# Kernel optimization log

Measured on AMD Instinct MI355X. Metric: run time of the kernel, lower is better.

## Reference

```python
import jax, jax.numpy as jnp
import numpy as np

N_NODES = 32
N_HEADS = 4
HEAD_DIM = 64
NEG_SLOPE = 0.2  # PyG GATConv default LeakyReLU slope


def setup_inputs() -> dict:
    key = jax.random.key(0)
    ks = jax.random.split(key, 8)
    roi_feats = jax.random.normal(ks[0], (N_NODES, 256, 96, 96), dtype=jnp.float32)
    edge_index = jax.random.randint(ks[1], (2, 512), 0, N_NODES, dtype=jnp.int32)
    W = jax.random.normal(ks[2], (256, N_HEADS * HEAD_DIM), dtype=jnp.float32) * 0.0625
    a_src = jax.random.normal(ks[3], (N_HEADS, HEAD_DIM), dtype=jnp.float32) * 0.125
    a_dst = jax.random.normal(ks[4], (N_HEADS, HEAD_DIM), dtype=jnp.float32) * 0.125
    gat_bias = jnp.zeros((N_HEADS * HEAD_DIM,), dtype=jnp.float32)
    cls_W = jax.random.normal(ks[5], (256, 32), dtype=jnp.float32) * 0.0625
    cls_b = jnp.zeros((32,), dtype=jnp.float32)
    return {"roi_feats": roi_feats, "edge_index": edge_index, "W": W,
            "a_src": a_src, "a_dst": a_dst, "gat_bias": gat_bias,
            "cls_W": cls_W, "cls_b": cls_b}


def _gat_conv(x, edge_index, W, a_src, a_dst, bias):
    # x: [N, C]; edge_index: [2, E] (src row 0, dst row 1)
    N = x.shape[0]
    # PyG GATConv adds self-loops by default
    loops = jnp.arange(N, dtype=edge_index.dtype)
    src = jnp.concatenate([edge_index[0], loops])
    dst = jnp.concatenate([edge_index[1], loops])
    h = (x @ W).reshape(N, N_HEADS, HEAD_DIM)          # [N, H, F]
    alpha_s = jnp.einsum('nhf,hf->nh', h, a_src)       # [N, H]
    alpha_d = jnp.einsum('nhf,hf->nh', h, a_dst)
    e = alpha_s[src] + alpha_d[dst]                    # [E', H]
    e = jnp.where(e >= 0, e, NEG_SLOPE * e)            # LeakyReLU
    # segment softmax over incoming edges of each dst node
    m = jax.ops.segment_max(e, dst, num_segments=N)    # [N, H]
    ex = jnp.exp(e - m[dst])
    denom = jax.ops.segment_sum(ex, dst, num_segments=N)
    alpha = ex / denom[dst]                            # [E', H]
    out = jax.ops.segment_sum(alpha[:, :, None] * h[src], dst, num_segments=N)
    return out.reshape(N, N_HEADS * HEAD_DIM) + bias


def reference(roi_feats, edge_index, W, a_src, a_dst, gat_bias, cls_W, cls_b):
    # [N, C, H, W] -> [N, C] spatial mean pool
    x = roi_feats.mean(axis=(2, 3))
    x = _gat_conv(x, edge_index, W, a_src, a_dst, gat_bias)
    logit = jax.nn.silu(x) @ cls_W + cls_b             # [N, num_au]
    return logit
```

## Files before the change

### kernel.cpp

```cpp
#include <hip/hip_runtime.h>
#include <math.h>

#define N_NODES  32
#define N_HEADS  4
#define HEAD_DIM 64
#define CDIM     256
#define HWPIX    9216
#define ROWF4    2304
#define E_BASE   512
#define E_TOT    544
#define NEG_SLOPE 0.2f
#define XS       257

__global__ __launch_bounds__(256, 4) void pool_kernel(const float* __restrict__ roi,
                                                      float* __restrict__ x) {
    const int wave = threadIdx.x >> 6, lane = threadIdx.x & 63;
    const int row = blockIdx.x * 4 + wave;
    const float4* p = reinterpret_cast<const float4*>(roi) + (size_t)row * ROWF4 + lane;

    float4 A[12], B[12];
    float s = 0.f;

#pragma unroll
    for (int j = 0; j < 12; ++j) A[j] = p[j * 64];
#pragma unroll
    for (int j = 0; j < 12; ++j) B[j] = p[(12 + j) * 64];
#pragma unroll
    for (int j = 0; j < 12; ++j) s += (A[j].x + A[j].y) + (A[j].z + A[j].w);
#pragma unroll
    for (int j = 0; j < 12; ++j) A[j] = p[(24 + j) * 64];
#pragma unroll
    for (int j = 0; j < 12; ++j) s += (B[j].x + B[j].y) + (B[j].z + B[j].w);
#pragma unroll
    for (int j = 0; j < 12; ++j) s += (A[j].x + A[j].y) + (A[j].z + A[j].w);

#pragma unroll
    for (int off = 32; off; off >>= 1) s += __shfl_down(s, off);
    if (lane == 0) x[row] = s * (1.0f / (float)HWPIX);
}

__global__ __launch_bounds__(256) void gat_kernel(const int* __restrict__ edge_index,
                                                  const float* __restrict__ x,
                                                  const float* __restrict__ W,
                                                  const float* __restrict__ a_src,
                                                  const float* __restrict__ a_dst,
                                                  const float* __restrict__ gat_bias,
                                                  const float* __restrict__ cls_W,
                                                  const float* __restrict__ cls_b,
                                                  float* __restrict__ out) {
    const int n = blockIdx.x;
    const int t = threadIdx.x;
    const int wavg = t >> 6, lane = t & 63;

    __shared__ float    xs[N_NODES * XS];
    __shared__ __align__(16) float asl[CDIM];
    __shared__ __align__(16) float adl[CDIM];
    __shared__ float    was[CDIM * N_HEADS];
    __shared__ float    wad[CDIM * N_HEADS];
    __shared__ float    als[N_NODES * N_HEADS];
    __shared__ float    adn[N_HEADS];
    __shared__ unsigned msegu[N_HEADS];
    __shared__ float    dseg[N_HEADS];
    __shared__ float    M[N_NODES * N_HEADS];
    __shared__ float    y[N_HEADS * CDIM];
    __shared__ float    sv[CDIM];
    __shared__ float4   red4[N_HEADS][64];
    __shared__ float    cred[8][32];

    float4 xv[8];
#pragma unroll
    for (int k = 0; k < 8; ++k) xv[k] = ((const float4*)x)[t + k * 256];
    const float asr = a_src[t], adr = a_dst[t];
    const int es0 = edge_index[t],       ed0 = edge_index[E_BASE + t];
    const int es1 = edge_index[256 + t], ed1 = edge_index[E_BASE + 256 + t];
    float4 bias4 = make_float4(0.f, 0.f, 0.f, 0.f);
    if (t < 64) bias4 = ((const float4*)gat_bias)[t];
    float cb = 0.f;
    if (t < 32) cb = cls_b[t];

#pragma unroll
    for (int k = 0; k < 8; ++k) {
        const int i = (t + k * 256) * 4, s = i >> 8, c = i & 255;
        xs[s * XS + c + 0] = xv[k].x;
        xs[s * XS + c + 1] = xv[k].y;
        xs[s * XS + c + 2] = xv[k].z;
        xs[s * XS + c + 3] = xv[k].w;
    }
    asl[t] = asr;
    adl[t] = adr;
    if (t < 128) M[t] = 0.f;
    if (t < 4) { msegu[t] = 0u; dseg[t] = 0.f; }
    __syncthreads();

    {
        float accs[4] = {0.f, 0.f, 0.f, 0.f};
        float accd[4] = {0.f, 0.f, 0.f, 0.f};
        const float4* wr  = (const float4*)(W + (size_t)t * CDIM);
        const float4* as4 = (const float4*)asl;
        const float4* ad4 = (const float4*)adl;
#pragma unroll 32
        for (int j = 0; j < 64; ++j) {
            const float4 w = wr[j], av = as4[j], dv = ad4[j];
            const int hd = j >> 4;
            accs[hd] += w.x * av.x + w.y * av.y + w.z * av.z + w.w * av.w;
            accd[hd] += w.x * dv.x + w.y * dv.y + w.z * dv.z + w.w * dv.w;
        }
#pragma unroll
        for (int hd = 0; hd < 4; ++hd) {
            was[t * 4 + hd] = accs[hd];
            wad[t * 4 + hd] = accd[hd];
        }
    }
    __syncthreads();

    if (t < 132) {
        if (t < 128) {
            const int s = t >> 2, hd = t & 3;
            const float* xrow = &xs[s * XS];
            float acc = 0.f;
#pragma unroll 8
            for (int c = 0; c < CDIM; ++c) acc += xrow[c] * was[c * 4 + hd];
            als[t] = acc;
        } else {
            const int hd = t - 128;
            const float* xrow = &xs[n * XS];
            float acc = 0.f;
#pragma unroll 8
            for (int c = 0; c < CDIM; ++c) acc += xrow[c] * wad[c * 4 + hd];
            adn[hd] = acc;
        }
    }
    __syncthreads();

    {
        const bool sl = (t < 32) && (t == n);
#pragma unroll
        for (int hd = 0; hd < 4; ++hd) {
            float best = -INFINITY;
            if (ed0 == n) {
                float v = als[es0 * 4 + hd] + adn[hd];
                best = fmaxf(best, (v >= 0.f) ? v : NEG_SLOPE * v);
            }
            if (ed1 == n) {
                float v = als[es1 * 4 + hd] + adn[hd];
                best = fmaxf(best, (v >= 0.f) ? v : NEG_SLOPE * v);
            }
            if (sl) {
                float v = als[n * 4 + hd] + adn[hd];
                best = fmaxf(best, (v >= 0.f) ? v : NEG_SLOPE * v);
            }
            if (best > -INFINITY) {
                const int iv = __float_as_int(best);
                const unsigned key = (iv < 0) ? ~(unsigned)iv
                                              : ((unsigned)iv | 0x80000000u);
                atomicMax(&msegu[hd], key);
            }
        }
    }
    __syncthreads();

    float mx[4];
#pragma unroll
    for (int hd = 0; hd < 4; ++hd) {
        const unsigned key = msegu[hd];
        const int im = (key & 0x80000000u) ? (int)(key & 0x7fffffffu) : (int)~key;
        mx[hd] = __int_as_float(im);
    }

    {
        const bool sl = (t < 32) && (t == n);
#pragma unroll
        for (int hd = 0; hd < 4; ++hd) {
            if (ed0 == n) {
                float v = als[es0 * 4 + hd] + adn[hd];
                v = (v >= 0.f) ? v : NEG_SLOPE * v;
                const float ex = expf(v - mx[hd]);
                atomicAdd(&dseg[hd], ex);
                atomicAdd(&M[es0 * 4 + hd], ex);
            }
            if (ed1 == n) {
                float v = als[es1 * 4 + hd] + adn[hd];
                v = (v >= 0.f) ? v : NEG_SLOPE * v;
                const float ex = expf(v - mx[hd]);
                atomicAdd(&dseg[hd], ex);
                atomicAdd(&M[es1 * 4 + hd], ex);
            }
            if (sl) {
                float v = als[n * 4 + hd] + adn[hd];
                v = (v >= 0.f) ? v : NEG_SLOPE * v;
                const float ex = expf(v - mx[hd]);
                atomicAdd(&dseg[hd], ex);
                atomicAdd(&M[n * 4 + hd], ex);
            }
        }
    }
    __syncthreads();
    if (t < 128) M[t] /= dseg[t & 3];
    __syncthreads();

    {
        const int hd = wavg;
        float a0 = 0.f, a1 = 0.f, a2 = 0.f, a3 = 0.f;
#pragma unroll
        for (int s = 0; s < N_NODES; ++s) {
            const float m = M[s * 4 + hd];
            const float* xrow = &xs[s * XS + lane];
            a0 += m * xrow[0];   a1 += m * xrow[64];
            a2 += m * xrow[128]; a3 += m * xrow[192];
        }
        y[hd * CDIM + lane]       = a0;
        y[hd * CDIM + lane + 64]  = a1;
        y[hd * CDIM + lane + 128] = a2;
        y[hd * CDIM + lane + 192] = a3;
    }
    __syncthreads();

    {
        const int hd = lane >> 4;
        const float* yrow = &y[hd * CDIM];
        float4 acc = make_float4(0.f, 0.f, 0.f, 0.f);
#pragma unroll 16
        for (int cc = 0; cc < 64; ++cc) {
            const int c = wavg * 64 + cc;
            const float4 w4 = ((const float4*)(W + (size_t)c * CDIM))[lane];
            const float yv = yrow[c];
            acc.x += yv * w4.x; acc.y += yv * w4.y;
            acc.z += yv * w4.z; acc.w += yv * w4.w;
        }
        red4[wavg][lane] = acc;
    }
    __syncthreads();
    if (t < 64) {
        const float4 s0 = red4[0][t], s1 = red4[1][t];
        const float4 s2 = red4[2][t], s3 = red4[3][t];
        float v0 = s0.x + s1.x + s2.x + s3.x + bias4.x;
        float v1 = s0.y + s1.y + s2.y + s3.y + bias4.y;
        float v2 = s0.z + s1.z + s2.z + s3.z + bias4.z;
        float v3 = s0.w + s1.w + s2.w + s3.w + bias4.w;
        sv[4 * t + 0] = v0 / (1.0f + expf(-v0));
        sv[4 * t + 1] = v1 / (1.0f + expf(-v1));
        sv[4 * t + 2] = v2 / (1.0f + expf(-v2));
        sv[4 * t + 3] = v3 / (1.0f + expf(-v3));
    }
    __syncthreads();

    {
        const int j = t & 31, g8 = t >> 5;
        float a = 0.f;
#pragma unroll
        for (int c0 = 0; c0 < 32; ++c0) {
            const int c = g8 * 32 + c0;
            a += sv[c] * cls_W[c * 32 + j];
        }
        cred[g8][j] = a;
    }
    __syncthreads();
    if (t < 32) {
        float s2 = cb;
#pragma unroll
        for (int g2 = 0; g2 < 8; ++g2) s2 += cred[g2][t];
        out[n * 32 + t] = s2;
    }
}

extern "C" void kernel_launch(void* const* d_in, const int* in_sizes, int n_in,
                              void* d_out, int out_size, void* d_ws, size_t ws_size,
                              hipStream_t stream) {
    const float* roi   = (const float*)d_in[0];
    const int*   eidx  = (const int*)d_in[1];
    const float* W     = (const float*)d_in[2];
    const float* a_src = (const float*)d_in[3];
    const float* a_dst = (const float*)d_in[4];
    const float* gbias = (const float*)d_in[5];
    const float* clsW  = (const float*)d_in[6];
    const float* clsb  = (const float*)d_in[7];
    float* out = (float*)d_out;

    float* x = (float*)d_ws;

    pool_kernel<<<(N_NODES * CDIM) / 4, 256, 0, stream>>>(roi, x);
    gat_kernel<<<N_NODES, 256, 0, stream>>>(eidx, x, W, a_src, a_dst,
                                            gbias, clsW, clsb, out);
}
```

Baseline: 71.32 us.

## Compute H = xW once in a separate kernel instead of per-block refolding

```diff
diff --git a/kernel.cpp b/kernel.cpp
--- a/kernel.cpp
+++ b/kernel.cpp
@@ -3,7 +3,6 @@
 
 #define N_NODES  32
 #define N_HEADS  4
-#define HEAD_DIM 64
 #define CDIM     256
 #define HWPIX    9216
 #define ROWF4    2304
@@ -39,9 +38,38 @@
     if (lane == 0) x[row] = s * (1.0f / (float)HWPIX);
 }
 
+__global__ __launch_bounds__(256) void h_kernel(const float* __restrict__ x,
+                                                const float* __restrict__ W,
+                                                float* __restrict__ H) {
+    const int b = blockIdx.x;
+    const int s = b >> 3, colbase = (b & 7) * 32;
+    const int t = threadIdx.x;
+    __shared__ float xrow[CDIM];
+    __shared__ float part[8][32];
+
+    xrow[t] = x[s * CDIM + t];
+    __syncthreads();
+
+    const int j = t & 31, q = t >> 5;
+    const float* wp = W + (size_t)(q * 32) * CDIM + colbase + j;
+    const float* xq = &xrow[q * 32];
+    float acc = 0.f;
+#pragma unroll
+    for (int i = 0; i < 32; ++i)
+        acc += xq[i] * wp[(size_t)i * CDIM];
+    part[q][j] = acc;
+    __syncthreads();
+
+    if (t < 32) {
+        float a = 0.f;
+#pragma unroll
+        for (int qq = 0; qq < 8; ++qq) a += part[qq][t];
+        H[s * CDIM + colbase + t] = a;
+    }
+}
+
 __global__ __launch_bounds__(256) void gat_kernel(const int* __restrict__ edge_index,
-                                                  const float* __restrict__ x,
-                                                  const float* __restrict__ W,
+                                                  const float* __restrict__ H,
                                                   const float* __restrict__ a_src,
                                                   const float* __restrict__ a_dst,
                                                   const float* __restrict__ gat_bias,
@@ -50,83 +78,63 @@
                                                   float* __restrict__ out) {
     const int n = blockIdx.x;
     const int t = threadIdx.x;
-    const int wavg = t >> 6, lane = t & 63;
-
-    __shared__ float    xs[N_NODES * XS];
+
+    __shared__ float    hs[N_NODES * XS];
     __shared__ __align__(16) float asl[CDIM];
     __shared__ __align__(16) float adl[CDIM];
-    __shared__ float    was[CDIM * N_HEADS];
-    __shared__ float    wad[CDIM * N_HEADS];
     __shared__ float    als[N_NODES * N_HEADS];
     __shared__ float    adn[N_HEADS];
     __shared__ unsigned msegu[N_HEADS];
-    __shared__ float    dseg[N_HEADS];
     __shared__ float    M[N_NODES * N_HEADS];
-    __shared__ float    y[N_HEADS * CDIM];
     __shared__ float    sv[CDIM];
-    __shared__ float4   red4[N_HEADS][64];
     __shared__ float    cred[8][32];
 
-    float4 xv[8];
-#pragma unroll
-    for (int k = 0; k < 8; ++k) xv[k] = ((const float4*)x)[t + k * 256];
+    float4 hv[8];
+#pragma unroll
+    for (int k = 0; k < 8; ++k) hv[k] = ((const float4*)H)[t + k * 256];
     const float asr = a_src[t], adr = a_dst[t];
+    const float gb = gat_bias[t];
     const int es0 = edge_index[t],       ed0 = edge_index[E_BASE + t];
     const int es1 = edge_index[256 + t], ed1 = edge_index[E_BASE + 256 + t];
-    float4 bias4 = make_float4(0.f, 0.f, 0.f, 0.f);
-    if (t < 64) bias4 = ((const float4*)gat_bias)[t];
     float cb = 0.f;
     if (t < 32) cb = cls_b[t];
+    float cw[32];
+    {
+        const int j = t & 31, g = t >> 5;
+#pragma unroll
+        for (int i = 0; i < 32; ++i) cw[i] = cls_W[(g * 32 + i) * 32 + j];
+    }
 
 #pragma unroll
     for (int k = 0; k < 8; ++k) {
         const int i = (t + k * 256) * 4, s = i >> 8, c = i & 255;
-        xs[s * XS + c + 0] = xv[k].x;
-        xs[s * XS + c + 1] = xv[k].y;
-        xs[s * XS + c + 2] = xv[k].z;
-        xs[s * XS + c + 3] = xv[k].w;
+        hs[s * XS + c + 0] = hv[k].x;
+        hs[s * XS + c + 1] = hv[k].y;
+        hs[s * XS + c + 2] = hv[k].z;
+        hs[s * XS + c + 3] = hv[k].w;
     }
     asl[t] = asr;
     adl[t] = adr;
     if (t < 128) M[t] = 0.f;
-    if (t < 4) { msegu[t] = 0u; dseg[t] = 0.f; }
-    __syncthreads();
-
-    {
-        float accs[4] = {0.f, 0.f, 0.f, 0.f};
-        float accd[4] = {0.f, 0.f, 0.f, 0.f};
-        const float4* wr  = (const float4*)(W + (size_t)t * CDIM);
-        const float4* as4 = (const float4*)asl;
-        const float4* ad4 = (const float4*)adl;
-#pragma unroll 32
-        for (int j = 0; j < 64; ++j) {
-            const float4 w = wr[j], av = as4[j], dv = ad4[j];
-            const int hd = j >> 4;
-            accs[hd] += w.x * av.x + w.y * av.y + w.z * av.z + w.w * av.w;
-            accd[hd] += w.x * dv.x + w.y * dv.y + w.z * dv.z + w.w * dv.w;
-        }
-#pragma unroll
-        for (int hd = 0; hd < 4; ++hd) {
-            was[t * 4 + hd] = accs[hd];
-            wad[t * 4 + hd] = accd[hd];
-        }
-    }
+    if (t < 4)   msegu[t] = 0u;
     __syncthreads();
 
     if (t < 132) {
         if (t < 128) {
             const int s = t >> 2, hd = t & 3;
-            const float* xrow = &xs[s * XS];
+            const float* hrow = &hs[s * XS + hd * 64];
+            const float* av   = &asl[hd * 64];
             float acc = 0.f;
-#pragma unroll 8
-            for (int c = 0; c < CDIM; ++c) acc += xrow[c] * was[c * 4 + hd];
+#pragma unroll 16
+            for (int f = 0; f < 64; ++f) acc += hrow[f] * av[f];
             als[t] = acc;
         } else {
             const int hd = t - 128;
-            const float* xrow = &xs[n * XS];
+            const float* hrow = &hs[n * XS + hd * 64];
+            const float* av   = &adl[hd * 64];
             float acc = 0.f;
-#pragma unroll 8
-            for (int c = 0; c < CDIM; ++c) acc += xrow[c] * wad[c * 4 + hd];
+#pragma unroll 16
+            for (int f = 0; f < 64; ++f) acc += hrow[f] * av[f];
             adn[hd] = acc;
         }
     }
@@ -174,91 +182,48 @@
             if (ed0 == n) {
                 float v = als[es0 * 4 + hd] + adn[hd];
                 v = (v >= 0.f) ? v : NEG_SLOPE * v;
-                const float ex = expf(v - mx[hd]);
-                atomicAdd(&dseg[hd], ex);
-                atomicAdd(&M[es0 * 4 + hd], ex);
+                atomicAdd(&M[es0 * 4 + hd], expf(v - mx[hd]));
             }
             if (ed1 == n) {
                 float v = als[es1 * 4 + hd] + adn[hd];
                 v = (v >= 0.f) ? v : NEG_SLOPE * v;
-                const float ex = expf(v - mx[hd]);
-                atomicAdd(&dseg[hd], ex);
-                atomicAdd(&M[es1 * 4 + hd], ex);
+                atomicAdd(&M[es1 * 4 + hd], expf(v - mx[hd]));
             }
             if (sl) {
                 float v = als[n * 4 + hd] + adn[hd];
                 v = (v >= 0.f) ? v : NEG_SLOPE * v;
-                const float ex = expf(v - mx[hd]);
-                atomicAdd(&dseg[hd], ex);
-                atomicAdd(&M[n * 4 + hd], ex);
-            }
-        }
-    }
-    __syncthreads();
-    if (t < 128) M[t] /= dseg[t & 3];
-    __syncthreads();
-
-    {
-        const int hd = wavg;
-        float a0 = 0.f, a1 = 0.f, a2 = 0.f, a3 = 0.f;
+                atomicAdd(&M[n * 4 + hd], expf(v - mx[hd]));
+            }
+        }
+    }
+    __syncthreads();
+
+    {
+        const int hd = t >> 6;
+        float acc = 0.f, msum = 0.f;
 #pragma unroll
         for (int s = 0; s < N_NODES; ++s) {
             const float m = M[s * 4 + hd];
-            const float* xrow = &xs[s * XS + lane];
-            a0 += m * xrow[0];   a1 += m * xrow[64];
-            a2 += m * xrow[128]; a3 += m * xrow[192];
-        }
-        y[hd * CDIM + lane]       = a0;
-        y[hd * CDIM + lane + 64]  = a1;
-        y[hd * CDIM + lane + 128] = a2;
-        y[hd * CDIM + lane + 192] = a3;
-    }
-    __syncthreads();
-
-    {
-        const int hd = lane >> 4;
-        const float* yrow = &y[hd * CDIM];
-        float4 acc = make_float4(0.f, 0.f, 0.f, 0.f);
-#pragma unroll 16
-        for (int cc = 0; cc < 64; ++cc) {
-            const int c = wavg * 64 + cc;
-            const float4 w4 = ((const float4*)(W + (size_t)c * CDIM))[lane];
-            const float yv = yrow[c];
-            acc.x += yv * w4.x; acc.y += yv * w4.y;
-            acc.z += yv * w4.z; acc.w += yv * w4.w;
-        }
-        red4[wavg][lane] = acc;
-    }
-    __syncthreads();
-    if (t < 64) {
-        const float4 s0 = red4[0][t], s1 = red4[1][t];
-        const float4 s2 = red4[2][t], s3 = red4[3][t];
-        float v0 = s0.x + s1.x + s2.x + s3.x + bias4.x;
-        float v1 = s0.y + s1.y + s2.y + s3.y + bias4.y;
-        float v2 = s0.z + s1.z + s2.z + s3.z + bias4.z;
-        float v3 = s0.w + s1.w + s2.w + s3.w + bias4.w;
-        sv[4 * t + 0] = v0 / (1.0f + expf(-v0));
-        sv[4 * t + 1] = v1 / (1.0f + expf(-v1));
-        sv[4 * t + 2] = v2 / (1.0f + expf(-v2));
-        sv[4 * t + 3] = v3 / (1.0f + expf(-v3));
-    }
-    __syncthreads();
-
-    {
-        const int j = t & 31, g8 = t >> 5;
+            msum += m;
+            acc += m * hs[s * XS + t];
+        }
+        const float v = acc / msum + gb;
+        sv[t] = v / (1.0f + expf(-v));
+    }
+    __syncthreads();
+
+    {
+        const int j = t & 31, g = t >> 5;
         float a = 0.f;
 #pragma unroll
-        for (int c0 = 0; c0 < 32; ++c0) {
-            const int c = g8 * 32 + c0;
-            a += sv[c] * cls_W[c * 32 + j];
-        }
-        cred[g8][j] = a;
+        for (int i = 0; i < 32; ++i) a += sv[g * 32 + i] * cw[i];
+        cred[g][j] = a;
     }
     __syncthreads();
     if (t < 32) {
         float s2 = cb;
 #pragma unroll
-        for (int g2 = 0; g2 < 8; ++g2) s2 += cred[g2][t];
+        for (int g = 0; g < 8; ++g) s2 += cred[g][t];
         out[n * 32 + t] = s2;
     }
 }
@@ -277,8 +242,10 @@
     float* out = (float*)d_out;
 
     float* x = (float*)d_ws;
+    float* H = x + 8192;
 
     pool_kernel<<<(N_NODES * CDIM) / 4, 256, 0, stream>>>(roi, x);
-    gat_kernel<<<N_NODES, 256, 0, stream>>>(eidx, x, W, a_src, a_dst,
+    h_kernel<<<256, 256, 0, stream>>>(x, W, H);
+    gat_kernel<<<N_NODES, 256, 0, stream>>>(eidx, H, a_src, a_dst,
                                             gbias, clsW, clsb, out);
 }
```

Result: faster. 59.15 us (median of 2 runs) (-17.1%).
